# Kernel tuning notes

Measured on AMD Instinct MI355X. Metric: run time of the kernel, lower is better.

The kernel has to match this reference:

```python
import jax, jax.numpy as jnp
import numpy as np

CH = 1280
HEADS = 8
HEAD_DIM = 160
INNER = HEADS * HEAD_DIM  # 1280


def setup_inputs() -> dict:
    key = jax.random.key(0)
    ks = jax.random.split(key, 6)
    s = 1.0 / np.sqrt(CH)
    return {
        "hidden_states": jax.random.normal(ks[0], (2, 4096, CH), dtype=jnp.float32),
        "w_q": jax.random.normal(ks[1], (CH, INNER), dtype=jnp.float32) * s,
        "w_k": jax.random.normal(ks[2], (CH, INNER), dtype=jnp.float32) * s,
        "w_v": jax.random.normal(ks[3], (CH, INNER), dtype=jnp.float32) * s,
        "w_out": jax.random.normal(ks[4], (INNER, CH), dtype=jnp.float32) * (1.0 / np.sqrt(INNER)),
        "b_out": jax.random.normal(ks[5], (CH,), dtype=jnp.float32) * 0.01,
    }


def reference(hidden_states, w_q, w_k, w_v, w_out, b_out):
    B, S, C = hidden_states.shape
    scale = 1.0 / np.sqrt(HEAD_DIM)
    # self-attention: context = hidden_states
    q = (hidden_states @ w_q).reshape(B, S, HEADS, HEAD_DIM)
    k = (hidden_states @ w_k).reshape(B, S, HEADS, HEAD_DIM)
    v = (hidden_states @ w_v).reshape(B, S, HEADS, HEAD_DIM)
    # [B, H, S, S] explicit score matrix (matches original non-flash path)
    scores = jnp.einsum("bqhd,bkhd->bhqk", q, k) * scale
    attn = jax.nn.softmax(scores, axis=-1)
    out = jnp.einsum("bhqk,bkhd->bqhd", attn, v).reshape(B, S, INNER)
    return out @ w_out + b_out
```

## Files before the change

### kernel.cpp

```cpp
#include <hip/hip_runtime.h>
#include <hip/hip_bf16.h>
#include <stdint.h>


using bf16x8 = __attribute__((ext_vector_type(8))) short;
using f32x4  = __attribute__((ext_vector_type(4))) float;
using f32x16 = __attribute__((ext_vector_type(16))) float;

__device__ __forceinline__ short f2bf(float f) {
    union { float f; uint32_t u; } v; v.f = f;
    uint32_t r = v.u + 0x7fffu + ((v.u >> 16) & 1u);
    return (short)(r >> 16);
}

__device__ __forceinline__ void async16(const short* g, short* l) {
    __builtin_amdgcn_global_load_lds(
        (const __attribute__((address_space(1))) void*)g,
        (__attribute__((address_space(3))) void*)l, 16, 0, 0);
}

__global__ __launch_bounds__(256) void cast_hs(
    const float* __restrict__ hs, short* __restrict__ out)
{
    int i = (blockIdx.x * 256 + threadIdx.x) * 4;
    float4 v = *(const float4*)&hs[i];
    short4 s; s.x = f2bf(v.x); s.y = f2bf(v.y); s.z = f2bf(v.z); s.w = f2bf(v.w);
    *(short4*)&out[i] = s;
}

__global__ __launch_bounds__(256) void transpose_w(
    const float* __restrict__ w0, const float* __restrict__ w1,
    const float* __restrict__ w2, const float* __restrict__ w3,
    short* __restrict__ wqkvT, short* __restrict__ woutT)
{
    __shared__ float tile[32][33];
    int z = blockIdx.z;
    const float* src = (z == 0) ? w0 : (z == 1) ? w1 : (z == 2) ? w2 : w3;
    short* dst = (z == 3) ? woutT : (wqkvT + (long)z * 1280 * 1280);
    int k0 = blockIdx.x * 32, n0 = blockIdx.y * 32;
    int t = threadIdx.x, r = t >> 5, c = t & 31;
#pragma unroll
    for (int i = 0; i < 4; i++)
        tile[r + i * 8][c] = src[(long)(k0 + r + i * 8) * 1280 + n0 + c];
    __syncthreads();
#pragma unroll
    for (int i = 0; i < 4; i++)
        dst[(long)(n0 + r + i * 8) * 1280 + k0 + c] = f2bf(tile[c][r + i * 8]);
}

__global__ __launch_bounds__(256) void transpose_v(
    const short* __restrict__ v, short* __restrict__ vt)
{
    __shared__ short tile[32][33];
    int s0 = blockIdx.x * 32, d0 = blockIdx.y * 32;
    long bh = blockIdx.z;
    const short* src = v + bh * 4096 * 160;
    short* dst = vt + bh * 160 * 4096;
    int t = threadIdx.x, r = t >> 5, c = t & 31;
#pragma unroll
    for (int i = 0; i < 4; i++)
        tile[r + i * 8][c] = src[(s0 + r + i * 8) * 160 + d0 + c];
    __syncthreads();
#pragma unroll
    for (int i = 0; i < 4; i++)
        dst[(d0 + r + i * 8) * 4096 + s0 + c] = tile[c][r + i * 8];
}

template <int MODE>
__global__ __launch_bounds__(256, 3) void gemm_k(
    const short* __restrict__ A, const short* __restrict__ BT,
    short* __restrict__ q_h, short* __restrict__ k_h, short* __restrict__ v_h,
    float* __restrict__ outp, const float* __restrict__ bias)
{
    __shared__ __align__(16) short A_lds[128 * 64];
    __shared__ __align__(16) short B_lds[128 * 64];

    int t = threadIdx.x, wave = t >> 6, lane = t & 63;
    int quad = lane >> 4, l15 = lane & 15, h7 = l15 & 7;
    int wr = wave >> 1, wc = wave & 1;
    int m0 = blockIdx.y * 128, n0 = blockIdx.x * 128;

    f32x4 acc[4][4] = {};

    for (int kt = 0; kt < 1280; kt += 64) {
        __syncthreads();
#pragma unroll
        for (int i = 0; i < 4; i++) {
            int chunk = wave * 4 + i;
            int c = chunk * 64 + lane;
            int row = c >> 3, j = (c & 7) ^ (row & 7);
            async16(A  + (long)(m0 + row) * 1280 + kt + j * 8, A_lds + chunk * 512);
            async16(BT + (long)(n0 + row) * 1280 + kt + j * 8, B_lds + chunk * 512);
        }
        __syncthreads();

#pragma unroll
        for (int dk = 0; dk < 2; dk++) {
            bf16x8 a[4], b[4];
#pragma unroll
            for (int mi = 0; mi < 4; mi++) {
                int row = wr * 64 + mi * 16 + l15;
                a[mi] = *(const bf16x8*)&A_lds[row * 64 + ((dk * 4 + quad) ^ h7) * 8];
            }
#pragma unroll
            for (int ni = 0; ni < 4; ni++) {
                int row = wc * 64 + ni * 16 + l15;
                b[ni] = *(const bf16x8*)&B_lds[row * 64 + ((dk * 4 + quad) ^ h7) * 8];
            }
#pragma unroll
            for (int mi = 0; mi < 4; mi++)
#pragma unroll
                for (int ni = 0; ni < 4; ni++)
                    acc[mi][ni] = __builtin_amdgcn_mfma_f32_16x16x32_bf16(
                        a[mi], b[ni], acc[mi][ni], 0, 0, 0);
        }
    }

    const float SL2E = 0.07905694150420949f * 1.4426950408889634f;
#pragma unroll
    for (int mi = 0; mi < 4; mi++) {
#pragma unroll
        for (int ni = 0; ni < 4; ni++) {
#pragma unroll
            for (int r = 0; r < 4; r++) {
                int gr = m0 + wr * 64 + mi * 16 + quad * 4 + r;
                int gc = n0 + wc * 64 + ni * 16 + l15;
                float val = acc[mi][ni][r];
                if (MODE == 0) {
                    int which = gc / 1280;
                    int c1 = gc - which * 1280;
                    int hh = c1 / 160, d = c1 - hh * 160;
                    int b_ = gr >> 12, s = gr & 4095;
                    long addr = (((long)(b_ * 8 + hh)) * 4096 + s) * 160 + d;
                    if (which == 0) val *= SL2E;
                    short* dst = (which == 0) ? q_h : (which == 1) ? k_h : v_h;
                    dst[addr] = f2bf(val);
                } else {
                    outp[(long)gr * 1280 + gc] = val + bias[gc];
                }
            }
        }
    }
}

__global__ __launch_bounds__(256, 2) void flash_k(
    const short* __restrict__ q_h, const short* __restrict__ k_h,
    const short* __restrict__ v_t, short* __restrict__ attn_out)
{
    __shared__ __align__(16) short Ks128[64 * 128];
    __shared__ __align__(16) short Ks32 [64 * 32];
    __shared__ __align__(16) short Vs   [160 * 64];

    int t = threadIdx.x, wave = t >> 6, lane = t & 63;
    int l31 = lane & 31, hi = lane >> 5;
    int qt = blockIdx.x;
    long bh = blockIdx.y;
    int b = (int)(bh >> 3), h = (int)(bh & 7);

    bf16x8 qf[10];
    {
        const short* qg = q_h + (bh * 4096 + qt * 128 + wave * 32 + l31) * 160;
#pragma unroll
        for (int dk = 0; dk < 10; dk++)
            qf[dk] = *(const bf16x8*)&qg[dk * 16 + hi * 8];
    }

    auto stageK = [&](int k0) {
        const short* kg = k_h + (bh * 4096 + k0) * 160;
#pragma unroll
        for (int i = 0; i < 4; i++) {
            int chunk = wave * 4 + i;
            int c = chunk * 64 + lane;
            int row = c >> 4, j = (c & 15) ^ (row & 7);
            async16(kg + row * 160 + j * 8, Ks128 + chunk * 512);
        }
        {
            int row = wave * 16 + (lane >> 2);
            int r31 = row & 31;
            int j = (lane & 3) ^ (((r31 >> 1) & 3) ^ ((r31 >> 3) & 3));
            async16(kg + row * 160 + 128 + j * 8, Ks32 + wave * 512);
        }
    };
    auto stageV = [&](int k0) {
#pragma unroll
        for (int i = 0; i < 5; i++) {
            int chunk = wave * 5 + i;
            int c = chunk * 64 + lane;
            int row = c >> 3, j = (c & 7) ^ (row & 7);
            async16(v_t + (bh * 160 + row) * 4096 + k0 + j * 8, Vs + chunk * 512);
        }
    };

    f32x16 o[5] = {};
    float lacc = 0.f;
    int sk31 = ((l31 >> 1) & 3) ^ ((l31 >> 3) & 3);

    stageK(0);
    stageV(0);
    asm volatile("s_waitcnt vmcnt(5)" ::: "memory");
    asm volatile("s_waitcnt lgkmcnt(0)" ::: "memory");
    __builtin_amdgcn_s_barrier();

    for (int k0 = 0; k0 < 4096; k0 += 64) {
        uint32_t pw[4][4];

#pragma unroll
        for (int kt = 0; kt < 2; kt++) {
            f32x16 sa = {}, sb = {};
            __builtin_amdgcn_s_setprio(1);
#pragma unroll
            for (int dk = 0; dk < 8; dk += 2) {
                bf16x8 ka0 = *(const bf16x8*)
                    &Ks128[(kt * 32 + l31) * 128 + (((dk * 2 + hi) ^ (l31 & 7)) * 8)];
                bf16x8 ka1 = *(const bf16x8*)
                    &Ks128[(kt * 32 + l31) * 128 + ((((dk + 1) * 2 + hi) ^ (l31 & 7)) * 8)];
                sa = __builtin_amdgcn_mfma_f32_32x32x16_bf16(ka0, qf[dk],     sa, 0, 0, 0);
                sb = __builtin_amdgcn_mfma_f32_32x32x16_bf16(ka1, qf[dk + 1], sb, 0, 0, 0);
            }
            {
                bf16x8 ka8 = *(const bf16x8*)
                    &Ks32[(kt * 32 + l31) * 32 + (((0 * 2 + hi) ^ sk31) * 8)];
                bf16x8 ka9 = *(const bf16x8*)
                    &Ks32[(kt * 32 + l31) * 32 + (((1 * 2 + hi) ^ sk31) * 8)];
                sa = __builtin_amdgcn_mfma_f32_32x32x16_bf16(ka8, qf[8], sa, 0, 0, 0);
                sb = __builtin_amdgcn_mfma_f32_32x32x16_bf16(ka9, qf[9], sb, 0, 0, 0);
            }
            __builtin_amdgcn_s_setprio(0);
            f32x16 s = sa + sb;

            uint32_t u[4][2];
#pragma unroll
            for (int rg = 0; rg < 4; rg++) {
                float e0 = exp2f(s[rg * 4 + 0] - 16.f);
                float e1 = exp2f(s[rg * 4 + 1] - 16.f);
                float e2 = exp2f(s[rg * 4 + 2] - 16.f);
                float e3 = exp2f(s[rg * 4 + 3] - 16.f);
                uint32_t pk0, pk1;
                asm("v_cvt_pk_bf16_f32 %0, %1, %2" : "=v"(pk0) : "v"(e0), "v"(e1));
                asm("v_cvt_pk_bf16_f32 %0, %1, %2" : "=v"(pk1) : "v"(e2), "v"(e3));
                u[rg][0] = pk0; u[rg][1] = pk1;
                lacc += (e0 + e1) + (e2 + e3);
            }
#pragma unroll
            for (int ksl = 0; ksl < 2; ksl++)
#pragma unroll
                for (int c = 0; c < 2; c++) {
                    auto r = __builtin_amdgcn_permlane32_swap(
                        u[2 * ksl][c], u[2 * ksl + 1][c], false, false);
                    pw[kt * 2 + ksl][c]     = (uint32_t)r[0];
                    pw[kt * 2 + ksl][c + 2] = (uint32_t)r[1];
                }
        }

        asm volatile("s_waitcnt vmcnt(0)" ::: "memory");
        asm volatile("s_waitcnt lgkmcnt(0)" ::: "memory");
        __builtin_amdgcn_s_barrier();

        if (k0 + 64 < 4096) stageK(k0 + 64);

        __builtin_amdgcn_s_setprio(1);
#pragma unroll
        for (int ks = 0; ks < 4; ks++) {
            union { uint32_t w[4]; bf16x8 v; } ap;
            ap.w[0] = pw[ks][0]; ap.w[1] = pw[ks][1];
            ap.w[2] = pw[ks][2]; ap.w[3] = pw[ks][3];
#pragma unroll
            for (int ct = 0; ct < 5; ct++) {
                int row = ct * 32 + l31;
                bf16x8 bv = *(const bf16x8*)
                    &Vs[row * 64 + (((ks * 2 + hi) ^ (row & 7)) * 8)];
                o[ct] = __builtin_amdgcn_mfma_f32_32x32x16_bf16(ap.v, bv, o[ct], 0, 0, 0);
            }
        }
        __builtin_amdgcn_s_setprio(0);

        asm volatile("s_waitcnt vmcnt(0)" ::: "memory");
        asm volatile("s_waitcnt lgkmcnt(0)" ::: "memory");
        __builtin_amdgcn_s_barrier();

        if (k0 + 64 < 4096) stageV(k0 + 64);
    }

    float lsum = lacc + __shfl_xor(lacc, 32);
    float inv = 1.0f / lsum;
    float iv[16];
#pragma unroll
    for (int r = 0; r < 16; r++)
        iv[r] = __shfl(inv, (r & 3) + 8 * (r >> 2) + 4 * hi);

#pragma unroll
    for (int ct = 0; ct < 5; ct++)
#pragma unroll
        for (int r = 0; r < 16; r++) {
            int crow = (r & 3) + 8 * (r >> 2) + 4 * hi;
            int gr = b * 4096 + qt * 128 + wave * 32 + crow;
            int gc = h * 160 + ct * 32 + l31;
            attn_out[(long)gr * 1280 + gc] = f2bf(o[ct][r] * iv[r]);
        }
}

extern "C" void kernel_launch(void* const* d_in, const int* in_sizes, int n_in,
                              void* d_out, int out_size, void* d_ws, size_t ws_size,
                              hipStream_t stream)
{
    const float* hs = (const float*)d_in[0];
    const float* wq = (const float*)d_in[1];
    const float* wk = (const float*)d_in[2];
    const float* wv = (const float*)d_in[3];
    const float* wo = (const float*)d_in[4];
    const float* bo = (const float*)d_in[5];
    float* out = (float*)d_out;

    char* ws = (char*)d_ws;
    short* wqkvT = (short*)(ws + 0);
    short* woutT = (short*)(ws + 9830400);
    short* q_h   = (short*)(ws + 13107200);
    short* k_h   = (short*)(ws + 34078720);
    short* v_t   = (short*)(ws + 55050240);
    short* v_h   = (short*)(ws + 76021760);
    short* attn  = v_h;
    short* hs_bf = v_t;

    cast_hs<<<10240, 256, 0, stream>>>(hs, hs_bf);
    transpose_w<<<dim3(40, 40, 4), 256, 0, stream>>>(wq, wk, wv, wo, wqkvT, woutT);
    gemm_k<0><<<dim3(30, 64), 256, 0, stream>>>(hs_bf, wqkvT, q_h, k_h, v_h,
                                                nullptr, nullptr);
    transpose_v<<<dim3(128, 5, 16), 256, 0, stream>>>(v_h, v_t);
    flash_k<<<dim3(32, 16), 256, 0, stream>>>(q_h, k_h, v_t, attn);
    gemm_k<1><<<dim3(10, 64), 256, 0, stream>>>(attn, woutT, nullptr, nullptr,
                                                nullptr, out, bo);
}
```

Baseline: 453.7 us.

## Split KV sequence across two wave groups in flash attention and merge via LDS

Doubles the flash attention block to 512 threads so that two groups of four waves each process half of the key/value sequence for the same 128 query rows. Each group stages its own K/V tiles, and at the end the partial outputs and row sums are combined through LDS before normalization and store. This raises the number of waves in flight (512 blocks on a 256-CU part previously gave low occupancy) at the cost of extra LDS use, barriers, and a reduction step. Because softmax uses a fixed offset rather than a running max, the partial results can be added directly.

```diff
diff --git a/kernel.cpp b/kernel.cpp
--- a/kernel.cpp
+++ b/kernel.cpp
@@ -143,51 +143,56 @@
     }
 }
 
-__global__ __launch_bounds__(256, 2) void flash_k(
+__global__ __launch_bounds__(512, 4) void flash_k(
     const short* __restrict__ q_h, const short* __restrict__ k_h,
     const short* __restrict__ v_t, short* __restrict__ attn_out)
 {
-    __shared__ __align__(16) short Ks128[64 * 128];
-    __shared__ __align__(16) short Ks32 [64 * 32];
-    __shared__ __align__(16) short Vs   [160 * 64];
+    __shared__ __align__(16) short LDS[40960];
 
     int t = threadIdx.x, wave = t >> 6, lane = t & 63;
     int l31 = lane & 31, hi = lane >> 5;
+    int qw = wave & 3, kvh = wave >> 2;
     int qt = blockIdx.x;
     long bh = blockIdx.y;
     int b = (int)(bh >> 3), h = (int)(bh & 7);
 
+    short* Kb128 = LDS + kvh * 20480;
+    short* Kb32  = Kb128 + 8192;
+    short* Vb    = Kb128 + 10240;
+    long kbase = bh * 4096 + kvh * 2048;
+
     bf16x8 qf[10];
     {
-        const short* qg = q_h + (bh * 4096 + qt * 128 + wave * 32 + l31) * 160;
+        const short* qg = q_h + (bh * 4096 + qt * 128 + qw * 32 + l31) * 160;
 #pragma unroll
         for (int dk = 0; dk < 10; dk++)
             qf[dk] = *(const bf16x8*)&qg[dk * 16 + hi * 8];
     }
 
     auto stageK = [&](int k0) {
-        const short* kg = k_h + (bh * 4096 + k0) * 160;
+        const short* kg = k_h + (kbase + k0) * 160;
 #pragma unroll
         for (int i = 0; i < 4; i++) {
-            int chunk = wave * 4 + i;
+            int chunk = qw * 4 + i;
             int c = chunk * 64 + lane;
             int row = c >> 4, j = (c & 15) ^ (row & 7);
-            async16(kg + row * 160 + j * 8, Ks128 + chunk * 512);
+            async16(kg + row * 160 + j * 8, Kb128 + chunk * 512);
         }
         {
-            int row = wave * 16 + (lane >> 2);
+            int row = qw * 16 + (lane >> 2);
             int r31 = row & 31;
             int j = (lane & 3) ^ (((r31 >> 1) & 3) ^ ((r31 >> 3) & 3));
-            async16(kg + row * 160 + 128 + j * 8, Ks32 + wave * 512);
+            async16(kg + row * 160 + 128 + j * 8, Kb32 + qw * 512);
         }
     };
     auto stageV = [&](int k0) {
 #pragma unroll
         for (int i = 0; i < 5; i++) {
-            int chunk = wave * 5 + i;
+            int chunk = qw * 5 + i;
             int c = chunk * 64 + lane;
             int row = c >> 3, j = (c & 7) ^ (row & 7);
-            async16(v_t + (bh * 160 + row) * 4096 + k0 + j * 8, Vs + chunk * 512);
+            async16(v_t + (bh * 160 + row) * 4096 + (kvh * 2048 + k0) + j * 8,
+                    Vb + chunk * 512);
         }
     };
 
@@ -201,7 +206,7 @@
     asm volatile("s_waitcnt lgkmcnt(0)" ::: "memory");
     __builtin_amdgcn_s_barrier();
 
-    for (int k0 = 0; k0 < 4096; k0 += 64) {
+    for (int k0 = 0; k0 < 2048; k0 += 64) {
         uint32_t pw[4][4];
 
 #pragma unroll
@@ -211,17 +216,17 @@
 #pragma unroll
             for (int dk = 0; dk < 8; dk += 2) {
                 bf16x8 ka0 = *(const bf16x8*)
-                    &Ks128[(kt * 32 + l31) * 128 + (((dk * 2 + hi) ^ (l31 & 7)) * 8)];
+                    &Kb128[(kt * 32 + l31) * 128 + (((dk * 2 + hi) ^ (l31 & 7)) * 8)];
                 bf16x8 ka1 = *(const bf16x8*)
-                    &Ks128[(kt * 32 + l31) * 128 + ((((dk + 1) * 2 + hi) ^ (l31 & 7)) * 8)];
+                    &Kb128[(kt * 32 + l31) * 128 + ((((dk + 1) * 2 + hi) ^ (l31 & 7)) * 8)];
                 sa = __builtin_amdgcn_mfma_f32_32x32x16_bf16(ka0, qf[dk],     sa, 0, 0, 0);
                 sb = __builtin_amdgcn_mfma_f32_32x32x16_bf16(ka1, qf[dk + 1], sb, 0, 0, 0);
             }
             {
                 bf16x8 ka8 = *(const bf16x8*)
-                    &Ks32[(kt * 32 + l31) * 32 + (((0 * 2 + hi) ^ sk31) * 8)];
+                    &Kb32[(kt * 32 + l31) * 32 + (((0 * 2 + hi) ^ sk31) * 8)];
                 bf16x8 ka9 = *(const bf16x8*)
-                    &Ks32[(kt * 32 + l31) * 32 + (((1 * 2 + hi) ^ sk31) * 8)];
+                    &Kb32[(kt * 32 + l31) * 32 + (((1 * 2 + hi) ^ sk31) * 8)];
                 sa = __builtin_amdgcn_mfma_f32_32x32x16_bf16(ka8, qf[8], sa, 0, 0, 0);
                 sb = __builtin_amdgcn_mfma_f32_32x32x16_bf16(ka9, qf[9], sb, 0, 0, 0);
             }
@@ -256,7 +261,7 @@
         asm volatile("s_waitcnt lgkmcnt(0)" ::: "memory");
         __builtin_amdgcn_s_barrier();
 
-        if (k0 + 64 < 4096) stageK(k0 + 64);
+        if (k0 + 64 < 2048) stageK(k0 + 64);
 
         __builtin_amdgcn_s_setprio(1);
 #pragma unroll
@@ -268,7 +273,7 @@
             for (int ct = 0; ct < 5; ct++) {
                 int row = ct * 32 + l31;
                 bf16x8 bv = *(const bf16x8*)
-                    &Vs[row * 64 + (((ks * 2 + hi) ^ (row & 7)) * 8)];
+                    &Vb[row * 64 + (((ks * 2 + hi) ^ (row & 7)) * 8)];
                 o[ct] = __builtin_amdgcn_mfma_f32_32x32x16_bf16(ap.v, bv, o[ct], 0, 0, 0);
             }
         }
@@ -278,25 +283,61 @@
         asm volatile("s_waitcnt lgkmcnt(0)" ::: "memory");
         __builtin_amdgcn_s_barrier();
 
-        if (k0 + 64 < 4096) stageV(k0 + 64);
+        if (k0 + 64 < 2048) stageV(k0 + 64);
     }
 
     float lsum = lacc + __shfl_xor(lacc, 32);
-    float inv = 1.0f / lsum;
-    float iv[16];
-#pragma unroll
-    for (int r = 0; r < 16; r++)
-        iv[r] = __shfl(inv, (r & 3) + 8 * (r >> 2) + 4 * hi);
-
-#pragma unroll
-    for (int ct = 0; ct < 5; ct++)
-#pragma unroll
-        for (int r = 0; r < 16; r++) {
-            int crow = (r & 3) + 8 * (r >> 2) + 4 * hi;
-            int gr = b * 4096 + qt * 128 + wave * 32 + crow;
-            int gc = h * 160 + ct * 32 + l31;
-            attn_out[(long)gr * 1280 + gc] = f2bf(o[ct][r] * iv[r]);
-        }
+
+    float* exL = (float*)LDS;
+    if (kvh == 1 && hi == 0) exL[qw * 32 + l31] = lsum;
+    asm volatile("s_waitcnt lgkmcnt(0)" ::: "memory");
+    __builtin_amdgcn_s_barrier();
+    float lsum_o = 0.f;
+    if (kvh == 0) lsum_o = exL[qw * 32 + l31];
+    asm volatile("s_waitcnt lgkmcnt(0)" ::: "memory");
+    __builtin_amdgcn_s_barrier();
+
+    float* exO = (float*)LDS;
+    if (kvh == 1) {
+#pragma unroll
+        for (int ct = 0; ct < 5; ct++)
+#pragma unroll
+            for (int rr = 0; rr < 4; rr++) {
+                int plane = ct * 4 + rr;
+                float4 v4 = { o[ct][rr * 4 + 0], o[ct][rr * 4 + 1],
+                              o[ct][rr * 4 + 2], o[ct][rr * 4 + 3] };
+                *(float4*)&exO[plane * 1024 + qw * 256 + lane * 4] = v4;
+            }
+    }
+    asm volatile("s_waitcnt lgkmcnt(0)" ::: "memory");
+    __builtin_amdgcn_s_barrier();
+
+    if (kvh == 0) {
+#pragma unroll
+        for (int ct = 0; ct < 5; ct++)
+#pragma unroll
+            for (int rr = 0; rr < 4; rr++) {
+                int plane = ct * 4 + rr;
+                float4 v4 = *(const float4*)&exO[plane * 1024 + qw * 256 + lane * 4];
+                o[ct][rr * 4 + 0] += v4.x; o[ct][rr * 4 + 1] += v4.y;
+                o[ct][rr * 4 + 2] += v4.z; o[ct][rr * 4 + 3] += v4.w;
+            }
+        float inv = 1.0f / (lsum + lsum_o);
+        float iv[16];
+#pragma unroll
+        for (int r = 0; r < 16; r++)
+            iv[r] = __shfl(inv, (r & 3) + 8 * (r >> 2) + 4 * hi);
+
+#pragma unroll
+        for (int ct = 0; ct < 5; ct++)
+#pragma unroll
+            for (int r = 0; r < 16; r++) {
+                int crow = (r & 3) + 8 * (r >> 2) + 4 * hi;
+                int gr = b * 4096 + qt * 128 + qw * 32 + crow;
+                int gc = h * 160 + ct * 32 + l31;
+                attn_out[(long)gr * 1280 + gc] = f2bf(o[ct][r] * iv[r]);
+            }
+    }
 }
 
 extern "C" void kernel_launch(void* const* d_in, const int* in_sizes, int n_in,
@@ -326,7 +367,7 @@
     gemm_k<0><<<dim3(30, 64), 256, 0, stream>>>(hs_bf, wqkvT, q_h, k_h, v_h,
                                                 nullptr, nullptr);
     transpose_v<<<dim3(128, 5, 16), 256, 0, stream>>>(v_h, v_t);
-    flash_k<<<dim3(32, 16), 256, 0, stream>>>(q_h, k_h, v_t, attn);
+    flash_k<<<dim3(32, 16), 512, 0, stream>>>(q_h, k_h, v_t, attn);
     gemm_k<1><<<dim3(10, 64), 256, 0, stream>>>(attn, woutT, nullptr, nullptr,
                                                 nullptr, out, bo);
 }
```

After: 1.713 ms. 3.78x slower.
